# Optimization experiments

Measured on AMD Instinct MI355X. Metric: run time of the kernel, lower is better.

The kernel has to match this reference:

```python
import math
import jax, jax.numpy as jnp
import numpy as np

HID = 2048      # hidden_size
NH = 16         # num_heads
KD = HID // NH  # key head dim = 128 (even, required by XPOS)
VD = HID        # value_dim (value_factor=1)
VHD = VD // NH  # value head dim
SCALE_BASE = 512
ROPE_BASE = 10000.0
GN_EPS = 1e-5


def _rotate_every_two(x):
    x1 = x[..., ::2]
    x2 = x[..., 1::2]
    return jnp.stack((-x2, x1), axis=-1).reshape(x.shape)


def _dup(a):  # repeat_interleave(x, 2, dim=-1)
    return jnp.repeat(a, 2, axis=-1)


def _xpos_apply(x, pos, inv_freq, xpos_scale, downscale):
    # x: [B, H, S, KD], pos: [B, S]
    posf = pos.astype(jnp.float32)
    angles = posf[:, :, None] * inv_freq[None, None, :]          # [B, S, KD/2]
    sin = _dup(jnp.sin(angles))[:, None]                          # [B, 1, S, KD]
    cos = _dup(jnp.cos(angles))[:, None]
    scale = xpos_scale[None, None, :] ** (posf[:, :, None] / SCALE_BASE)
    if downscale:
        scale = 1.0 / scale
    scale = _dup(scale)[:, None]                                  # [B, 1, S, KD]
    return (x * cos + _rotate_every_two(x) * sin) * scale


def setup_inputs() -> dict:
    key = jax.random.key(0)
    ks = jax.random.split(key, 6)
    B, S = 1, 2048
    std = 1.0 / HID
    x = jax.random.normal(ks[0], (B, S, HID), dtype=jnp.float32)
    position_ids = jnp.broadcast_to(jnp.arange(S, dtype=jnp.int64), (B, S))
    Wq = jax.random.normal(ks[1], (HID, HID), dtype=jnp.float32) * std
    Wk = jax.random.normal(ks[2], (HID, HID), dtype=jnp.float32) * std
    Wv = jax.random.normal(ks[3], (HID, VD), dtype=jnp.float32) * std
    Wg = jax.random.normal(ks[4], (HID, VD), dtype=jnp.float32) * std
    Wo = jax.random.normal(ks[5], (VD, HID), dtype=jnp.float32) * std
    gn_weight = jnp.ones((VD,), dtype=jnp.float32)
    gn_bias = jnp.zeros((VD,), dtype=jnp.float32)
    return {"x": x, "position_ids": position_ids, "Wq": Wq, "Wk": Wk,
            "Wv": Wv, "Wg": Wg, "Wo": Wo,
            "gn_weight": gn_weight, "gn_bias": gn_bias}


def reference(x, position_ids, Wq, Wk, Wv, Wg, Wo, gn_weight, gn_bias):
    B, S, _ = x.shape
    # XPOS / multiscale-decay buffers (deterministic, as in XPOSRelativePosition)
    inv_freq = 1.0 / (ROPE_BASE ** (jnp.arange(0, KD, 2, dtype=jnp.float32) / KD))
    xpos_scale = (jnp.arange(0, KD, 2, dtype=jnp.float32) + 0.4 * KD) / (1.4 * KD)
    gamma = 1.0 - jnp.exp(jnp.linspace(math.log(1.0 / 32), math.log(1.0 / 512), NH))
    log_gamma = jnp.log(gamma)                                    # [NH]

    # projections -> [B, H, S, d]
    q = (x @ Wq).reshape(B, S, NH, KD).transpose(0, 2, 1, 3)
    k = (x @ Wk).reshape(B, S, NH, KD).transpose(0, 2, 1, 3)
    v = (x @ Wv).reshape(B, S, NH, VHD).transpose(0, 2, 1, 3)
    g = x @ Wg                                                    # [B, S, VD]

    q = _xpos_apply(q, position_ids, inv_freq, xpos_scale, downscale=False)
    k = _xpos_apply(k, position_ids, inv_freq, xpos_scale, downscale=True)

    # decay mask: exp(log_gamma * (i-j)) for i>=j else 0   [B, H, S, S]
    relpos = position_ids[:, :, None] - position_ids[:, None, :]  # [B, S, S]
    decay = jnp.exp(log_gamma[None, :, None, None]
                    * jnp.maximum(relpos, 0)[:, None].astype(jnp.float32))
    decay = decay * (relpos >= 0)[:, None].astype(jnp.float32)

    scores = jnp.einsum('bhqd,bhkd->bhqk', q, k) * decay          # [B, H, S, S]
    retained = jnp.einsum('bhqk,bhkv->bhqv', scores, v)           # [B, H, S, VHD]

    # GroupNorm(num_heads, value_dim): normalize each head group per token
    r = retained.transpose(0, 2, 1, 3)                            # [B, S, H, VHD]
    mean = r.mean(axis=-1, keepdims=True)
    var = r.var(axis=-1, keepdims=True)
    rn = (r - mean) * jax.lax.rsqrt(var + GN_EPS)
    rn = rn * gn_weight.reshape(NH, VHD) + gn_bias.reshape(NH, VHD)
    rn = rn.reshape(B, S, VD)

    out = (jax.nn.silu(g) * rn) @ Wo                              # [B, S, HID]
    return out
```

## Files before the change

### kernel.cpp

```cpp
#include <hip/hip_runtime.h>
#include <math.h>

#define S_LEN 2048
#define HIDD  2048
#define NHEAD 16
#define HD    128

#define TILE_SH 4096

typedef __attribute__((ext_vector_type(8))) short short8;
typedef __attribute__((ext_vector_type(4))) float float4v;
typedef unsigned short ushort_t;

static __device__ __forceinline__ ushort_t f2bf(float f) {
    unsigned int u = __float_as_uint(f);
    u += 0x7fff + ((u >> 16) & 1);
    return (ushort_t)(u >> 16);
}
static __device__ __forceinline__ float bf2f(ushort_t s) {
    return __uint_as_float(((unsigned int)s) << 16);
}
__device__ __forceinline__ float silu_f(float x) { return x / (1.f + expf(-x)); }

__device__ __forceinline__ void gl_lds16(const ushort_t* g, short* l) {
    __builtin_amdgcn_global_load_lds((const __attribute__((address_space(1))) void*)g,
                                     (__attribute__((address_space(3))) void*)l, 16, 0, 0);
}

__global__ __launch_bounds__(256)
void split_kernel(const float* __restrict__ in, ushort_t* __restrict__ hi,
                  ushort_t* __restrict__ lo, int n4)
{
    const int i = blockIdx.x * 256 + threadIdx.x;
    if (i >= n4) return;
    const float4 v = ((const float4*)in)[i];
    ushort4 h, l;
    h.x = f2bf(v.x); l.x = f2bf(v.x - bf2f(h.x));
    h.y = f2bf(v.y); l.y = f2bf(v.y - bf2f(h.y));
    h.z = f2bf(v.z); l.z = f2bf(v.z - bf2f(h.z));
    h.w = f2bf(v.w); l.w = f2bf(v.w - bf2f(h.w));
    const int row = i >> 9, c4 = (i & 511) * 4;
    const size_t off = ((size_t)((row >> 7) * 64 + (c4 >> 5))) * TILE_SH
                     + (row & 127) * 32 + (c4 & 31);
    *(ushort4*)&hi[off] = h;
    *(ushort4*)&lo[off] = l;
}

__global__ __launch_bounds__(256)
void addp_kernel(float* __restrict__ out, const float* __restrict__ p, int n4)
{
    const int i = blockIdx.x * 256 + threadIdx.x;
    if (i >= n4) return;
    float4 a = ((const float4*)out)[i];
    const float4 b = ((const float4*)p)[i];
    a.x += b.x; a.y += b.y; a.z += b.z; a.w += b.w;
    ((float4*)out)[i] = a;
}

__global__ __launch_bounds__(256)
void split_transpose(const float* __restrict__ W, ushort_t* __restrict__ Thi,
                     ushort_t* __restrict__ Tlo)
{
    __shared__ float t[64][65];
    const int k0 = blockIdx.y * 64, n0 = blockIdx.x * 64;
    const int tx = threadIdx.x & 15, ty = threadIdx.x >> 4;
    #pragma unroll
    for (int it = 0; it < 4; it++) {
        const int k = ty + it * 16;
        const float4 v = *(const float4*)&W[(size_t)(k0 + k) * HIDD + n0 + tx * 4];
        t[k][tx * 4 + 0] = v.x; t[k][tx * 4 + 1] = v.y;
        t[k][tx * 4 + 2] = v.z; t[k][tx * 4 + 3] = v.w;
    }
    __syncthreads();
    #pragma unroll
    for (int it = 0; it < 4; it++) {
        const int n = ty + it * 16;
        ushort4 h, l; float a;
        a = t[tx * 4 + 0][n]; h.x = f2bf(a); l.x = f2bf(a - bf2f(h.x));
        a = t[tx * 4 + 1][n]; h.y = f2bf(a); l.y = f2bf(a - bf2f(h.y));
        a = t[tx * 4 + 2][n]; h.z = f2bf(a); l.z = f2bf(a - bf2f(h.z));
        a = t[tx * 4 + 3][n]; h.w = f2bf(a); l.w = f2bf(a - bf2f(h.w));
        const int nn_ = n0 + n, kk_ = k0 + tx * 4;
        const size_t off = ((size_t)((nn_ >> 7) * 64 + (kk_ >> 5))) * TILE_SH
                         + (nn_ & 127) * 32 + (kk_ & 31);
        *(ushort4*)&Thi[off] = h;
        *(ushort4*)&Tlo[off] = l;
    }
}

template<int MODE>
__global__ __launch_bounds__(256, 2)
void mfma_gemm(const ushort_t* __restrict__ Ahi, const ushort_t* __restrict__ Alo,
               const ushort_t* __restrict__ WT, const int* __restrict__ pos_ids,
               ushort_t* __restrict__ qhi, ushort_t* __restrict__ qlo,
               ushort_t* __restrict__ khi, ushort_t* __restrict__ klo,
               ushort_t* __restrict__ vThi, ushort_t* __restrict__ vTlo,
               float* __restrict__ gbuf, float* __restrict__ outC)
{
    __shared__ __align__(16) short sm[16384];

    const int tid = threadIdx.x;
    const int w = tid >> 6, L = tid & 63;
    const int qd = L >> 4, lc = L & 15;
    const int lin = blockIdx.x;
    int n0, m0, kh = 0;
    if (MODE == 0) {
        n0 = (((lin & 7) << 3) + ((lin >> 3) & 7)) << 7;
        m0 = (lin >> 6) << 7;
    } else {
        n0 = (lin & 15) << 7;
        m0 = ((lin >> 4) & 15) << 7;
        kh = lin >> 8;
    }
    const size_t PL = (size_t)HIDD * HIDD;

    int sel, nn;
    const ushort_t *Bhi, *Blo;
    if (MODE == 0) {
        sel = n0 >> 11; nn = n0 & 2047;
        Bhi = WT + (size_t)sel * 2 * PL; Blo = Bhi + PL;
    } else {
        sel = -1; nn = n0;
        Bhi = WT; Blo = WT + PL;
    }

    const ushort_t* pbase = (w == 0) ? Ahi : (w == 1) ? Alo : (w == 2) ? Bhi : Blo;
    const int rt = ((w < 2) ? m0 : nn) >> 7;
    const ushort_t* tb0 = pbase + (size_t)rt * 64 * TILE_SH + L * 8;
    short* ldsw = sm + w * 4096;

    const int wm = (w & 1) * 64, wn = (w >> 1) * 64;
    int aoff[4], boff[4];
    #pragma unroll
    for (int i = 0; i < 4; i++) aoff[i] = (wm + i * 16 + lc) * 32 + qd * 8;
    #pragma unroll
    for (int j = 0; j < 4; j++) boff[j] = (wn + j * 16 + lc) * 32 + qd * 8;

    float4v acc[4][4];
    #pragma unroll
    for (int i = 0; i < 4; i++)
        #pragma unroll
        for (int j = 0; j < 4; j++)
            #pragma unroll
            for (int r = 0; r < 4; r++) acc[i][j][r] = 0.f;

    const int kt0 = (MODE == 1) ? kh * 32 : 0;
    const int kt1 = (MODE == 1) ? kt0 + 32 : 64;
    for (int kt = kt0; kt < kt1; kt++) {
        const ushort_t* g = tb0 + (size_t)kt * TILE_SH;
        #pragma unroll
        for (int t = 0; t < 8; t++)
            gl_lds16(g + t * 512, ldsw + t * 512);
        __syncthreads();

        short8 bhf[4], blf[4];
        #pragma unroll
        for (int j = 0; j < 4; j++) {
            bhf[j] = *(const short8*)(sm + 8192  + boff[j]);
            blf[j] = *(const short8*)(sm + 12288 + boff[j]);
        }
        #pragma unroll
        for (int i = 0; i < 4; i++) {
            const short8 ahf = *(const short8*)(sm + aoff[i]);
            const short8 alf = *(const short8*)(sm + 4096 + aoff[i]);
            #pragma unroll
            for (int j = 0; j < 4; j++) {
                acc[i][j] = __builtin_amdgcn_mfma_f32_16x16x32_bf16(ahf, bhf[j], acc[i][j], 0, 0, 0);
                acc[i][j] = __builtin_amdgcn_mfma_f32_16x16x32_bf16(alf, bhf[j], acc[i][j], 0, 0, 0);
                acc[i][j] = __builtin_amdgcn_mfma_f32_16x16x32_bf16(ahf, blf[j], acc[i][j], 0, 0, 0);
            }
        }
        __syncthreads();
    }

    float* ob = (float*)sm;
    const int half = w & 1;
    const int head = nn >> 7;

    #pragma unroll
    for (int i = 0; i < 4; i++) {
        #pragma unroll
        for (int j = 0; j < 4; j++)
            #pragma unroll
            for (int r = 0; r < 4; r++)
                ob[(half * 16 + qd * 4 + r) * 132 + wn + j * 16 + lc] = acc[i][j][r];
        __syncthreads();

        if (MODE == 1 || sel == 3) {
            float* dst = (MODE == 1) ? (kh ? gbuf : outC) : gbuf;
            #pragma unroll
            for (int p = 0; p < 4; p++) {
                const int row = p * 8 + (tid >> 5);
                const int c = (tid & 31) * 4;
                const int grow = m0 + (row >> 4) * 64 + i * 16 + (row & 15);
                const float4 vv = *(const float4*)&ob[row * 132 + c];
                *(float4*)&dst[(size_t)grow * HIDD + nn + c] = vv;
            }
        } else if (sel == 2) {
            const int d = tid >> 1, hs = tid & 1;
            const int sbase = m0 + hs * 64 + i * 16;
            short8 h0, h1, l0, l1;
            #pragma unroll
            for (int sp = 0; sp < 8; sp++) {
                float a = ob[(hs * 16 + sp) * 132 + d];
                ushort_t hb = f2bf(a);
                h0[sp] = (short)hb; l0[sp] = (short)f2bf(a - bf2f(hb));
                a = ob[(hs * 16 + 8 + sp) * 132 + d];
                hb = f2bf(a);
                h1[sp] = (short)hb; l1[sp] = (short)f2bf(a - bf2f(hb));
            }
            ushort_t* dh = vThi + ((size_t)head * HD + d) * S_LEN + sbase;
            ushort_t* dl = vTlo + ((size_t)head * HD + d) * S_LEN + sbase;
            *(short8*)dh = h0; *(short8*)(dh + 8) = h1;
            *(short8*)dl = l0; *(short8*)(dl + 8) = l1;
        } else {
            const float sgn = (sel == 0) ? 1.f : -1.f;
            ushort_t* dhb = (sel == 0) ? qhi : khi;
            ushort_t* dlb = (sel == 0) ? qlo : klo;
            #pragma unroll
            for (int p = 0; p < 2; p++) {
                const int row = p * 16 + (tid >> 4);
                const int c8 = (tid & 15) * 8;
                const int grow = m0 + (row >> 4) * 64 + i * 16 + (row & 15);
                const float pos = (float)pos_ids[grow];
                const float pe = sgn * pos * (1.f / 512.f);
                short8 hv, lv;
                #pragma unroll
                for (int pp = 0; pp < 4; pp++) {
                    const int d = c8 + pp * 2;
                    const float v0 = ob[row * 132 + d], v1 = ob[row * 132 + d + 1];
                    const float invf = exp2f(-(float)d * (13.28771238f / 128.f));
                    float s, c_; sincosf(pos * invf, &s, &c_);
                    const float scl = exp2f(log2f(((float)d + 51.2f) * (1.f / 179.2f)) * pe);
                    const float e0 = (v0 * c_ - v1 * s) * scl;
                    const float e1 = (v1 * c_ + v0 * s) * scl;
                    const ushort_t h0 = f2bf(e0), h1 = f2bf(e1);
                    hv[pp * 2] = (short)h0;  hv[pp * 2 + 1] = (short)h1;
                    lv[pp * 2] = (short)f2bf(e0 - bf2f(h0));
                    lv[pp * 2 + 1] = (short)f2bf(e1 - bf2f(h1));
                }
                *(short8*)&dhb[((size_t)head * S_LEN + grow) * HD + c8] = hv;
                *(short8*)&dlb[((size_t)head * S_LEN + grow) * HD + c8] = lv;
            }
        }
        __syncthreads();
    }
}

#define KROW 136
#define VROW 40
#define KH_  0
#define KL_  (32 * KROW)
#define VH_  (2 * 32 * KROW)
#define VL_  (VH_ + 128 * VROW)
#define PH_  (VH_ + 2 * 128 * VROW)
#define PLO_ (PH_ + 64 * VROW)
#define YH_  8704
#define YL_  (YH_ + 64 * KROW)
__global__ __launch_bounds__(256, 2)
void retention2(const ushort_t* __restrict__ qhi, const ushort_t* __restrict__ qlo,
                const ushort_t* __restrict__ khi, const ushort_t* __restrict__ klo,
                const ushort_t* __restrict__ vThi, const ushort_t* __restrict__ vTlo,
                const float* __restrict__ gbuf, const float* __restrict__ gnw,
                const float* __restrict__ gnb,
                ushort_t* __restrict__ yhi, ushort_t* __restrict__ ylo)
{
    __shared__ __align__(16) short sm[26112];

    const int h = blockIdx.y;
    const int qb = (gridDim.x - 1) - blockIdx.x;
    const int r0 = qb * 64;
    const int tid = threadIdx.x;
    const int w = tid >> 6, L = tid & 63;
    const int qd = L >> 4, lc = L & 15;

    const float e = -3.4657359f + (float)h * ((-6.2383246f + 3.4657359f) / 15.f);
    const float lg2g = logf(1.f - expf(e)) * 1.44269504f;

    short8 qfh[4], qfl[4];
    {
        const size_t qb0 = ((size_t)h * S_LEN + r0 + w * 16 + lc) * HD + qd * 8;
        #pragma unroll
        for (int ks = 0; ks < 4; ks++) {
            qfh[ks] = *(const short8*)(qhi + qb0 + ks * 32);
            qfl[ks] = *(const short8*)(qlo + qb0 + ks * 32);
        }
    }

    float4v osum[2][4];
    #pragma unroll
    for (int mt = 0; mt < 2; mt++)
        #pragma unroll
        for (int j = 0; j < 4; j++)
            #pragma unroll
            for (int r = 0; r < 4; r++) osum[mt][j][r] = 0.f;

    const int qh_ = w >> 1, vh_ = w & 1;
    const int nch = (r0 + 64) / 32;

    for (int ch = 0; ch < nch; ch++) {
        const int kg0 = ch * 32;
        #pragma unroll
        for (int t = 0; t < 4; t++) {
            const int c = t * 256 + tid;
            const int p = c >> 9, r = (c >> 4) & 31, qq = c & 15;
            const ushort_t* src = (p ? klo : khi) + ((size_t)h * S_LEN + kg0 + r) * HD + qq * 8;
            *(short8*)(sm + (p ? KL_ : KH_) + r * KROW + qq * 8) = *(const short8*)src;
        }
        #pragma unroll
        for (int t = 0; t < 4; t++) {
            const int c = t * 256 + tid;
            const int p = c >> 9, r = (c >> 2) & 127, qq = c & 3;
            const ushort_t* src = (p ? vTlo : vThi) + ((size_t)h * HD + r) * S_LEN + kg0 + qq * 8;
            *(short8*)(sm + (p ? VL_ : VH_) + r * VROW + qq * 8) = *(const short8*)src;
        }
        __syncthreads();

        float4v sacc[2];
        #pragma unroll
        for (int j = 0; j < 2; j++)
            #pragma unroll
            for (int r = 0; r < 4; r++) sacc[j][r] = 0.f;
        #pragma unroll
        for (int ks = 0; ks < 4; ks++) {
            #pragma unroll
            for (int j = 0; j < 2; j++) {
                const short8 bh = *(const short8*)(sm + KH_ + (j * 16 + lc) * KROW + ks * 32 + qd * 8);
                const short8 bl = *(const short8*)(sm + KL_ + (j * 16 + lc) * KROW + ks * 32 + qd * 8);
                sacc[j] = __builtin_amdgcn_mfma_f32_16x16x32_bf16(qfh[ks], bh, sacc[j], 0, 0, 0);
                sacc[j] = __builtin_amdgcn_mfma_f32_16x16x32_bf16(qfl[ks], bh, sacc[j], 0, 0, 0);
                sacc[j] = __builtin_amdgcn_mfma_f32_16x16x32_bf16(qfh[ks], bl, sacc[j], 0, 0, 0);
            }
        }
        #pragma unroll
        for (int j = 0; j < 2; j++)
            #pragma unroll
            for (int r = 0; r < 4; r++) {
                const int dq = (r0 + w * 16 + qd * 4 + r) - (kg0 + j * 16 + lc);
                const float p = (dq >= 0) ? sacc[j][r] * exp2f(lg2g * (float)dq) : 0.f;
                const ushort_t hb = f2bf(p);
                const int off = (w * 16 + qd * 4 + r) * VROW + j * 16 + lc;
                sm[PH_ + off]  = (short)hb;
                sm[PLO_ + off] = (short)f2bf(p - bf2f(hb));
            }
        __syncthreads();

        #pragma unroll
        for (int mt = 0; mt < 2; mt++) {
            const short8 pfh = *(const short8*)(sm + PH_  + (qh_ * 32 + mt * 16 + lc) * VROW + qd * 8);
            const short8 pfl = *(const short8*)(sm + PLO_ + (qh_ * 32 + mt * 16 + lc) * VROW + qd * 8);
            #pragma unroll
            for (int j = 0; j < 4; j++) {
                const short8 vfh = *(const short8*)(sm + VH_ + (vh_ * 64 + j * 16 + lc) * VROW + qd * 8);
                const short8 vfl = *(const short8*)(sm + VL_ + (vh_ * 64 + j * 16 + lc) * VROW + qd * 8);
                osum[mt][j] = __builtin_amdgcn_mfma_f32_16x16x32_bf16(pfh, vfh, osum[mt][j], 0, 0, 0);
                osum[mt][j] = __builtin_amdgcn_mfma_f32_16x16x32_bf16(pfl, vfh, osum[mt][j], 0, 0, 0);
                osum[mt][j] = __builtin_amdgcn_mfma_f32_16x16x32_bf16(pfh, vfl, osum[mt][j], 0, 0, 0);
            }
        }
        __syncthreads();
    }

    float* fr = (float*)sm;
    #pragma unroll
    for (int mt = 0; mt < 2; mt++)
        #pragma unroll
        for (int r = 0; r < 4; r++) {
            float s1 = 0.f, s2 = 0.f;
            #pragma unroll
            for (int j = 0; j < 4; j++) { const float v = osum[mt][j][r]; s1 += v; s2 += v * v; }
            const int row = qh_ * 32 + mt * 16 + qd * 4 + r;
            fr[row * 32 + vh_ * 16 + lc] = s1;
            fr[2048 + row * 32 + vh_ * 16 + lc] = s2;
        }
    __syncthreads();
    if (tid < 64) {
        float s1 = 0.f, s2 = 0.f;
        #pragma unroll
        for (int t = 0; t < 32; t++) { s1 += fr[tid * 32 + t]; s2 += fr[2048 + tid * 32 + t]; }
        const float mean = s1 * (1.f / 128.f);
        const float var  = s2 * (1.f / 128.f) - mean * mean;
        fr[4096 + tid] = mean;
        fr[4160 + tid] = 1.f / sqrtf(var + 1e-5f);
    }
    __syncthreads();

    #pragma unroll
    for (int mt = 0; mt < 2; mt++)
        #pragma unroll
        for (int r = 0; r < 4; r++) {
            const int row = qh_ * 32 + mt * 16 + qd * 4 + r;
            const float mean = fr[4096 + row], inv = fr[4160 + row];
            const int grow = r0 + row;
            #pragma unroll
            for (int j = 0; j < 4; j++) {
                const int col = vh_ * 64 + j * 16 + lc;
                const float gv = gbuf[(size_t)grow * HIDD + h * HD + col];
                const float o = ((osum[mt][j][r] - mean) * inv * gnw[h * HD + col]
                                 + gnb[h * HD + col]) * silu_f(gv);
                const ushort_t hb = f2bf(o);
                sm[YH_ + row * KROW + col] = (short)hb;
                sm[YL_ + row * KROW + col] = (short)f2bf(o - bf2f(hb));
            }
        }
    __syncthreads();
    {
        const int r_ = tid >> 2, cs = (tid & 3) * 32;
        const int grow = r0 + r_;
        const size_t tb = ((size_t)((grow >> 7) * 64 + h * 4 + (tid & 3))) * TILE_SH
                        + (grow & 127) * 32;
        #pragma unroll
        for (int c8 = 0; c8 < 4; c8++) {
            *(short8*)(yhi + tb + c8 * 8) = *(const short8*)(sm + YH_ + r_ * KROW + cs + c8 * 8);
            *(short8*)(ylo + tb + c8 * 8) = *(const short8*)(sm + YL_ + r_ * KROW + cs + c8 * 8);
        }
    }
}

extern "C" void kernel_launch(void* const* d_in, const int* in_sizes, int n_in,
                              void* d_out, int out_size, void* d_ws, size_t ws_size,
                              hipStream_t stream) {
    const float* x   = (const float*)d_in[0];
    const int*   pid = (const int*)d_in[1];
    const float* W[5] = {(const float*)d_in[2], (const float*)d_in[3], (const float*)d_in[4],
                         (const float*)d_in[5], (const float*)d_in[6]};
    const float* gnw = (const float*)d_in[7];
    const float* gnb = (const float*)d_in[8];
    float* out = (float*)d_out;
    (void)in_sizes; (void)n_in; (void)out_size; (void)ws_size;

    const size_t PL = (size_t)HIDD * HIDD;

    ushort_t* wt   = (ushort_t*)d_ws;
    ushort_t* xhi  = wt + 10 * PL;
    ushort_t* xlo  = xhi + PL;
    ushort_t* qhi_ = xlo + PL;
    ushort_t* qlo_ = qhi_ + PL;
    ushort_t* khi_ = qlo_ + PL;
    ushort_t* klo_ = khi_ + PL;
    ushort_t* vThi = klo_ + PL;
    ushort_t* vTlo = vThi + PL;
    float*    gbuf = (float*)(vTlo + PL);
    ushort_t* yhi  = (ushort_t*)(gbuf + PL);
    ushort_t* ylo  = yhi + PL;
    float*    p1   = (float*)xhi;

    split_kernel<<<(int)(PL / 4 / 256), 256, 0, stream>>>(x, xhi, xlo, (int)(PL / 4));
    for (int m = 0; m < 5; m++)
        split_transpose<<<dim3(32, 32), 256, 0, stream>>>(W[m], wt + (size_t)m * 2 * PL,
                                                          wt + (size_t)m * 2 * PL + PL);

    mfma_gemm<0><<<1024, 256, 0, stream>>>(xhi, xlo, wt, pid,
        qhi_, qlo_, khi_, klo_, vThi, vTlo, gbuf, nullptr);

    retention2<<<dim3(32, 16), 256, 0, stream>>>(qhi_, qlo_, khi_, klo_, vThi, vTlo,
        gbuf, gnw, gnb, yhi, ylo);

    mfma_gemm<1><<<512, 256, 0, stream>>>(yhi, ylo, wt + 8 * PL, pid,
        nullptr, nullptr, nullptr, nullptr, nullptr, nullptr, p1, out);

    addp_kernel<<<(int)(PL / 4 / 256), 256, 0, stream>>>(out, p1, (int)(PL / 4));
}
```

Baseline: 550.7 us.

## Double-buffer LDS tiles in split-bf16 MFMA GEMM and swizzle LDS layout

```diff
diff --git a/kernel.cpp b/kernel.cpp
--- a/kernel.cpp
+++ b/kernel.cpp
@@ -97,7 +97,7 @@
                ushort_t* __restrict__ vThi, ushort_t* __restrict__ vTlo,
                float* __restrict__ gbuf, float* __restrict__ outC)
 {
-    __shared__ __align__(16) short sm[16384];
+    __shared__ __align__(16) short sm[32768];
 
     const int tid = threadIdx.x;
     const int w = tid >> 6, L = tid & 63;
@@ -126,15 +126,16 @@
 
     const ushort_t* pbase = (w == 0) ? Ahi : (w == 1) ? Alo : (w == 2) ? Bhi : Blo;
     const int rt = ((w < 2) ? m0 : nn) >> 7;
-    const ushort_t* tb0 = pbase + (size_t)rt * 64 * TILE_SH + L * 8;
-    short* ldsw = sm + w * 4096;
+    const int lsw = ((L >> 2) * 32) + (((L & 3) ^ ((L >> 2) & 3)) * 8);
+    const ushort_t* tb0 = pbase + (size_t)rt * 64 * TILE_SH + lsw;
 
     const int wm = (w & 1) * 64, wn = (w >> 1) * 64;
+    const int sx = (qd ^ (lc & 3)) * 8;
     int aoff[4], boff[4];
     #pragma unroll
-    for (int i = 0; i < 4; i++) aoff[i] = (wm + i * 16 + lc) * 32 + qd * 8;
-    #pragma unroll
-    for (int j = 0; j < 4; j++) boff[j] = (wn + j * 16 + lc) * 32 + qd * 8;
+    for (int i = 0; i < 4; i++) aoff[i] = (wm + i * 16 + lc) * 32 + sx;
+    #pragma unroll
+    for (int j = 0; j < 4; j++) boff[j] = (wn + j * 16 + lc) * 32 + sx;
 
     float4v acc[4][4];
     #pragma unroll
@@ -146,23 +147,38 @@
 
     const int kt0 = (MODE == 1) ? kh * 32 : 0;
     const int kt1 = (MODE == 1) ? kt0 + 32 : 64;
+
+    {
+        const ushort_t* g = tb0 + (size_t)kt0 * TILE_SH;
+        #pragma unroll
+        for (int t = 0; t < 8; t++)
+            gl_lds16(g + t * 512, sm + w * 4096 + t * 512);
+        asm volatile("s_waitcnt vmcnt(0)" ::: "memory");
+        __builtin_amdgcn_s_barrier();
+        __builtin_amdgcn_sched_barrier(0);
+    }
+
+    int cur = 0;
     for (int kt = kt0; kt < kt1; kt++) {
-        const ushort_t* g = tb0 + (size_t)kt * TILE_SH;
-        #pragma unroll
-        for (int t = 0; t < 8; t++)
-            gl_lds16(g + t * 512, ldsw + t * 512);
-        __syncthreads();
+        const short* cb = sm + (cur << 14);
+        short* nb = sm + ((cur ^ 1) << 14);
+        if (kt + 1 < kt1) {
+            const ushort_t* g = tb0 + (size_t)(kt + 1) * TILE_SH;
+            #pragma unroll
+            for (int t = 0; t < 8; t++)
+                gl_lds16(g + t * 512, nb + w * 4096 + t * 512);
+        }
 
         short8 bhf[4], blf[4];
         #pragma unroll
         for (int j = 0; j < 4; j++) {
-            bhf[j] = *(const short8*)(sm + 8192  + boff[j]);
-            blf[j] = *(const short8*)(sm + 12288 + boff[j]);
+            bhf[j] = *(const short8*)(cb + 8192  + boff[j]);
+            blf[j] = *(const short8*)(cb + 12288 + boff[j]);
         }
         #pragma unroll
         for (int i = 0; i < 4; i++) {
-            const short8 ahf = *(const short8*)(sm + aoff[i]);
-            const short8 alf = *(const short8*)(sm + 4096 + aoff[i]);
+            const short8 ahf = *(const short8*)(cb + aoff[i]);
+            const short8 alf = *(const short8*)(cb + 4096 + aoff[i]);
             #pragma unroll
             for (int j = 0; j < 4; j++) {
                 acc[i][j] = __builtin_amdgcn_mfma_f32_16x16x32_bf16(ahf, bhf[j], acc[i][j], 0, 0, 0);
@@ -170,7 +186,11 @@
                 acc[i][j] = __builtin_amdgcn_mfma_f32_16x16x32_bf16(ahf, blf[j], acc[i][j], 0, 0, 0);
             }
         }
-        __syncthreads();
+
+        asm volatile("s_waitcnt vmcnt(0)" ::: "memory");
+        __builtin_amdgcn_s_barrier();
+        __builtin_amdgcn_sched_barrier(0);
+        cur ^= 1;
     }
 
     float* ob = (float*)sm;
```

New measurement: 535.5 us. 1.03x faster.
